# Kernel optimization log

Hardware: AMD Instinct MI355X
Metric: run time of the kernel (lower is better)

The kernel has to match this reference:

```python
import jax, jax.numpy as jnp
import numpy as np

EPS = 1e-5  # torch BatchNorm1d / LayerNorm default eps
B, S, CTX, C, H = 64, 31, 2048, 512, 8  # S must be num_particles+1 = 31
DH = C // H


def layernorm(x, g, b):
    mu = x.mean(-1, keepdims=True)
    var = x.var(-1, keepdims=True)
    return (x - mu) / jnp.sqrt(var + EPS) * g + b


def setup_inputs() -> dict:
    key = jax.random.key(0)
    ks = jax.random.split(key, 16)
    w = lambda k, shape: jax.random.normal(k, shape, jnp.float32) * 0.02
    return {
        "queries": jax.random.normal(ks[0], (B, S, C), jnp.float32),
        "contexts": jax.random.normal(ks[1], (B, CTX, C), jnp.float32),
        # SelfAttention params (BatchNorm1d(C) in training mode, q/k/v no bias, out with bias)
        "sa_bn_g": jnp.ones((C,), jnp.float32),
        "sa_bn_b": jnp.zeros((C,), jnp.float32),
        "sa_q_w": w(ks[2], (C, C)),
        "sa_k_w": w(ks[3], (C, C)),
        "sa_v_w": w(ks[4], (C, C)),
        "sa_out_w": w(ks[5], (C, C)),
        "sa_out_b": jnp.zeros((C,), jnp.float32),
        "sa_pre_g": jnp.ones((S * S,), jnp.float32),  # BatchNorm1d(961) on energy
        "sa_pre_b": jnp.zeros((S * S,), jnp.float32),
        # Cross Attention params (LayerNorm on queries, q/k/v no bias, out with bias)
        "ca_ln_g": jnp.ones((C,), jnp.float32),
        "ca_ln_b": jnp.zeros((C,), jnp.float32),
        "ca_q_w": w(ks[6], (C, C)),
        "ca_k_w": w(ks[7], (C, C)),
        "ca_v_w": w(ks[8], (C, C)),
        "ca_out_w": w(ks[9], (C, C)),
        "ca_out_b": jnp.zeros((C,), jnp.float32),
        # FFN: LN -> SiLU -> Linear(C,2C,no bias) -> LN -> SiLU -> Linear(2C,C,no bias)
        "ff_ln1_g": jnp.ones((C,), jnp.float32),
        "ff_ln1_b": jnp.zeros((C,), jnp.float32),
        "ff_w1": w(ks[10], (2 * C, C)),
        "ff_ln2_g": jnp.ones((2 * C,), jnp.float32),
        "ff_ln2_b": jnp.zeros((2 * C,), jnp.float32),
        "ff_w2": w(ks[11], (C, 2 * C)),
    }


def reference(queries, contexts, sa_bn_g, sa_bn_b, sa_q_w, sa_k_w, sa_v_w,
              sa_out_w, sa_out_b, sa_pre_g, sa_pre_b, ca_ln_g, ca_ln_b,
              ca_q_w, ca_k_w, ca_v_w, ca_out_w, ca_out_b, ff_ln1_g, ff_ln1_b,
              ff_w1, ff_ln2_g, ff_ln2_b, ff_w2):
    scale = jnp.sqrt(jnp.asarray(C, queries.dtype))

    # ---- SelfAttention (normalization='Batch', training-mode batch stats) ----
    mu = queries.mean(axis=(0, 1))            # per-channel over (B, S)
    var = queries.var(axis=(0, 1))
    xn = (queries - mu) / jnp.sqrt(var + EPS) * sa_bn_g + sa_bn_b
    q = jnp.einsum('bsc,oc->bso', xn, sa_q_w).reshape(B, S, H, DH)
    k = jnp.einsum('bsc,oc->bso', xn, sa_k_w).reshape(B, S, H, DH)
    v = jnp.einsum('bsc,oc->bso', xn, sa_v_w).reshape(B, S, H, DH)
    energy = jnp.einsum('nqhc,nkhc->nhqk', q, k)          # (B,H,S,S)
    # pre-softmax BatchNorm1d over channels = flattened (q,k) positions, batch dims = (B, H)
    e = energy.reshape(B, H, S * S)                        # (B,H,S*S)
    mu2 = e.mean(axis=(0, 1))
    var2 = e.var(axis=(0, 1))
    en = (e - mu2) / jnp.sqrt(var2 + EPS) * sa_pre_g + sa_pre_b
    energy_post = en.reshape(B, H, S, S)
    attn = jax.nn.softmax(energy_post / scale, axis=-1)
    o = jnp.einsum('nhql,nlhc->nqhc', attn, v).reshape(B, S, C)
    o = jnp.einsum('bsc,oc->bso', o, sa_out_w) + sa_out_b
    x_sa = o + queries                                     # residual

    # ---- Cross Attention (LayerNorm on queries pre-projection) ----
    qn = layernorm(x_sa, ca_ln_g, ca_ln_b)
    q2 = jnp.einsum('bsc,oc->bso', qn, ca_q_w).reshape(B, S, H, DH)
    k2 = jnp.einsum('btc,oc->bto', contexts, ca_k_w).reshape(B, CTX, H, DH)
    v2 = jnp.einsum('btc,oc->bto', contexts, ca_v_w).reshape(B, CTX, H, DH)
    energy2 = jnp.einsum('nqhc,nkhc->nhqk', q2, k2)        # (B,H,S,CTX)
    attn2 = jax.nn.softmax(energy2 / scale, axis=-1)
    o2 = jnp.einsum('nhql,nlhc->nqhc', attn2, v2).reshape(B, S, C)
    o2 = jnp.einsum('bsc,oc->bso', o2, ca_out_w) + ca_out_b
    x_ca = o2 + x_sa                                       # residual (queries_pre)

    # ---- FFN: LN -> SiLU -> Linear -> LN -> SiLU -> Linear, + residual ----
    h = jax.nn.silu(layernorm(x_ca, ff_ln1_g, ff_ln1_b))
    h = jnp.einsum('bsc,oc->bso', h, ff_w1)                # (B,S,2C)
    h = jax.nn.silu(layernorm(h, ff_ln2_g, ff_ln2_b))
    h = jnp.einsum('bsc,oc->bso', h, ff_w2)                # (B,S,C)
    out = x_ca + h                                         # dropout p=0.0 -> identity
    return out, energy2
```

## Files before the change

kernel.cpp:

```cpp
#include <hip/hip_runtime.h>
#include <hip/hip_bf16.h>
#include <cstdint>
#include <cstddef>

using u16 = unsigned short;
typedef short short8 __attribute__((ext_vector_type(8)));
typedef short short4v __attribute__((ext_vector_type(4)));
typedef float f32x4  __attribute__((ext_vector_type(4)));

#define DEV static __device__ __forceinline__

DEV float b2f(u16 u){ union{ unsigned i; float f; } v; v.i = ((unsigned)u)<<16; return v.f; }
DEV u16 f2b(float f){
  unsigned i = __builtin_bit_cast(unsigned, f);
  unsigned r = (i + 0x7FFFu + ((i>>16)&1u)) >> 16;
  return (u16)r;
}
DEV f32x4 mfma16(short8 a, short8 b, f32x4 c){
  return __builtin_amdgcn_mfma_f32_16x16x32_bf16(a, b, c, 0, 0, 0);
}

constexpr int Bn=64, Sn=31, Tn=2048, Cn=512, Hn=8;
constexpr int Rn=Bn*Sn;
constexpr int BHn=Bn*Hn;
constexpr int HRn=Hn*Sn;
constexpr float EPSf=1e-5f;
constexpr float INV_SCALE=0.04419417382415922f;

__global__ void k_badorder(float* out){
  if(threadIdx.x==0) out[0]=2000.f;
}

struct Src8 { const float* p[8]; };
__global__ __launch_bounds__(256) void k_cvtall(Src8 s, u16* __restrict__ dst){
  int i = blockIdx.x*256 + threadIdx.x;
  int seg, j=i;
  if(j>=196608){ if(j>=262144){seg=7;j-=262144;} else {seg=6;j-=196608;} }
  else { seg=j>>15; j&=32767; }
  const float* src=s.p[seg];
  f32x4 a=*(const f32x4*)&src[(size_t)j*8];
  f32x4 b=*(const f32x4*)&src[(size_t)j*8+4];
  short8 o;
  #pragma unroll
  for(int q=0;q<4;++q){ o[q]=(short)f2b(a[q]); o[4+q]=(short)f2b(b[q]); }
  *(short8*)&dst[(size_t)i*8]=o;
}

__global__ __launch_bounds__(256) void k_bn1_partial(const float* __restrict__ q,
    float* __restrict__ ps, float* __restrict__ psq){
  int c = blockIdx.x*256 + threadIdx.x;
  int r0 = blockIdx.y*124;
  float s=0.f, sq=0.f;
  for(int r=r0; r<r0+124; ++r){ float v=q[(size_t)r*Cn+c]; s+=v; sq+=v*v; }
  ps [blockIdx.y*Cn+c]=s;
  psq[blockIdx.y*Cn+c]=sq;
}
__global__ __launch_bounds__(512) void k_bn1_final(const float* __restrict__ ps,
    const float* __restrict__ psq, const float* __restrict__ g,
    const float* __restrict__ b, float* __restrict__ scale, float* __restrict__ shift){
  int c = threadIdx.x;
  float s=0.f, sq=0.f;
  for(int i=0;i<16;++i){ s+=ps[i*Cn+c]; sq+=psq[i*Cn+c]; }
  float m = s/(float)Rn;
  float v = sq/(float)Rn - m*m;
  float rs = rsqrtf(v+EPSf);
  float sc = rs*g[c];
  scale[c]=sc; shift[c]=b[c]-m*sc;
}

__global__ __launch_bounds__(256) void k_qkv(
    const float* __restrict__ q, const float* __restrict__ scale,
    const float* __restrict__ shift,
    const u16* __restrict__ W0, const u16* __restrict__ W1, const u16* __restrict__ W2,
    u16* __restrict__ o0, u16* __restrict__ o1v, u16* __restrict__ o2v)
{
  __shared__ u16 As[64][72];
  __shared__ u16 Ws[64][72];
  const int z=blockIdx.z;
  const u16* W = (z==0)?W0:((z==1)?W1:W2);
  u16* out     = (z==0)?o0:((z==1)?o1v:o2v);
  const int t=threadIdx.x, w=t>>6, l=t&63;
  const int m0=blockIdx.x*64, n0=blockIdx.y*64;
  const int lr=l&15, lk=(l>>4)*8;
  f32x4 zero={0.f,0.f,0.f,0.f};
  f32x4 acc[4];
  #pragma unroll
  for(int i=0;i<4;++i) acc[i]=zero;
  const int row0=t>>3, c8=(t&7)*8;
  for(int k0=0;k0<Cn;k0+=64){
    f32x4 sc0=*(const f32x4*)&scale[k0+c8], sc1=*(const f32x4*)&scale[k0+c8+4];
    f32x4 sh0=*(const f32x4*)&shift[k0+c8], sh1=*(const f32x4*)&shift[k0+c8+4];
    f32x4 x00=*(const f32x4*)&q[(size_t)(m0+row0   )*Cn+k0+c8];
    f32x4 x01=*(const f32x4*)&q[(size_t)(m0+row0   )*Cn+k0+c8+4];
    f32x4 x10=*(const f32x4*)&q[(size_t)(m0+32+row0)*Cn+k0+c8];
    f32x4 x11=*(const f32x4*)&q[(size_t)(m0+32+row0)*Cn+k0+c8+4];
    short8 a0,a1;
    #pragma unroll
    for(int j=0;j<4;++j){
      a0[j]  =(short)f2b(fmaf(x00[j],sc0[j],sh0[j]));
      a0[4+j]=(short)f2b(fmaf(x01[j],sc1[j],sh1[j]));
      a1[j]  =(short)f2b(fmaf(x10[j],sc0[j],sh0[j]));
      a1[4+j]=(short)f2b(fmaf(x11[j],sc1[j],sh1[j]));
    }
    short8 w0=*(const short8*)&W[(size_t)(n0+row0   )*Cn + k0 + c8];
    short8 w1=*(const short8*)&W[(size_t)(n0+32+row0)*Cn + k0 + c8];
    __syncthreads();
    *(short8*)&As[row0   ][c8]=a0;
    *(short8*)&As[32+row0][c8]=a1;
    *(short8*)&Ws[row0   ][c8]=w0;
    *(short8*)&Ws[32+row0][c8]=w1;
    __syncthreads();
    #pragma unroll
    for(int ks=0;ks<64;ks+=32){
      short8 af=*(const short8*)&As[w*16+lr][ks+lk];
      #pragma unroll
      for(int nf=0;nf<4;++nf){
        short8 bf=*(const short8*)&Ws[nf*16+lr][ks+lk];
        acc[nf]=mfma16(af,bf,acc[nf]);
      }
    }
  }
  const int r0=w*16+(l>>4)*4;
  #pragma unroll
  for(int nf=0;nf<4;++nf){
    const int n=n0+nf*16+lr;
    #pragma unroll
    for(int r=0;r<4;++r){
      const int m=m0+r0+r;
      out[(size_t)m*Cn+n]=f2b(acc[nf][r]);
    }
  }
}

template<bool F32OUT, bool RES32>
__global__ __launch_bounds__(256) void k_gemm64(
    const u16* __restrict__ A, const u16* __restrict__ W,
    const float* __restrict__ bias, const void* __restrict__ res,
    void* __restrict__ outv, int M, int N, int K)
{
  __shared__ u16 As[64][72];
  __shared__ u16 Ws[64][72];
  const int t=threadIdx.x, w=t>>6, l=t&63;
  const int m0=blockIdx.x*64, n0=blockIdx.y*64;
  const int lr=l&15, lk=(l>>4)*8;
  f32x4 zero={0.f,0.f,0.f,0.f};
  f32x4 acc[4];
  #pragma unroll
  for(int i=0;i<4;++i) acc[i]=zero;
  const int row0=t>>3, c8=(t&7)*8;
  for(int k0=0;k0<K;k0+=64){
    short8 a0=*(const short8*)&A[(size_t)(m0+row0   )*K + k0 + c8];
    short8 a1=*(const short8*)&A[(size_t)(m0+32+row0)*K + k0 + c8];
    short8 w0=*(const short8*)&W[(size_t)(n0+row0   )*K + k0 + c8];
    short8 w1=*(const short8*)&W[(size_t)(n0+32+row0)*K + k0 + c8];
    __syncthreads();
    *(short8*)&As[row0   ][c8]=a0;
    *(short8*)&As[32+row0][c8]=a1;
    *(short8*)&Ws[row0   ][c8]=w0;
    *(short8*)&Ws[32+row0][c8]=w1;
    __syncthreads();
    #pragma unroll
    for(int ks=0;ks<64;ks+=32){
      short8 af=*(const short8*)&As[w*16+lr][ks+lk];
      #pragma unroll
      for(int nf=0;nf<4;++nf){
        short8 bf=*(const short8*)&Ws[nf*16+lr][ks+lk];
        acc[nf]=mfma16(af,bf,acc[nf]);
      }
    }
  }
  const int r0=w*16+(l>>4)*4;
  #pragma unroll
  for(int nf=0;nf<4;++nf){
    const int n=n0+nf*16+lr;
    float bv = bias? bias[n] : 0.f;
    #pragma unroll
    for(int r=0;r<4;++r){
      const int m=m0+r0+r;
      float vv=acc[nf][r]+bv;
      if(res){
        if(RES32) vv += ((const float*)res)[(size_t)m*N+n];
        else      vv += b2f(((const u16*)res)[(size_t)m*N+n]);
      }
      if(F32OUT) ((float*)outv)[(size_t)m*N+n]=vv;
      else       ((u16*)outv)[(size_t)m*N+n]=f2b(vv);
    }
  }
}

__global__ __launch_bounds__(64) void k_energy1(const u16* __restrict__ q,
    const u16* __restrict__ k, float* __restrict__ e1){
  __shared__ u16 qs[32][72];
  __shared__ u16 ks_[32][72];
  const int bh=blockIdx.x, b=bh>>3, h=bh&7;
  const int t=threadIdx.x, l=t;
  #pragma unroll
  for(int i=0;i<4;++i){
    int flat=i*64+t; int row=flat>>3, c8=(flat&7)*8;
    short8 zq={0,0,0,0,0,0,0,0}, zk={0,0,0,0,0,0,0,0};
    if(row<31){
      zq=*(const short8*)&q[(size_t)(b*31+row)*Cn + h*64 + c8];
      zk=*(const short8*)&k[(size_t)(b*31+row)*Cn + h*64 + c8];
    }
    *(short8*)&qs [row][c8]=zq;
    *(short8*)&ks_[row][c8]=zk;
  }
  __syncthreads();
  const int lr=l&15, lk=(l>>4)*8;
  f32x4 zero={0.f,0.f,0.f,0.f};
  f32x4 acc[2][2];
  acc[0][0]=zero; acc[0][1]=zero; acc[1][0]=zero; acc[1][1]=zero;
  #pragma unroll
  for(int ks=0;ks<64;ks+=32){
    short8 a0=*(const short8*)&qs [lr   ][ks+lk];
    short8 a1=*(const short8*)&qs [16+lr][ks+lk];
    short8 b0=*(const short8*)&ks_[lr   ][ks+lk];
    short8 b1=*(const short8*)&ks_[16+lr][ks+lk];
    acc[0][0]=mfma16(a0,b0,acc[0][0]);
    acc[0][1]=mfma16(a0,b1,acc[0][1]);
    acc[1][0]=mfma16(a1,b0,acc[1][0]);
    acc[1][1]=mfma16(a1,b1,acc[1][1]);
  }
  const int r0=(l>>4)*4;
  #pragma unroll
  for(int i=0;i<2;++i)
    #pragma unroll
    for(int j=0;j<2;++j)
      #pragma unroll
      for(int r=0;r<4;++r){
        int qi=i*16+r0+r, ki=j*16+lr;
        if(qi<31 && ki<31) e1[(size_t)bh*961 + qi*31 + ki]=acc[i][j][r];
      }
}

__global__ __launch_bounds__(256) void k_bn2_partial(const float* __restrict__ e1,
    float* __restrict__ ps, float* __restrict__ psq){
  int p=blockIdx.x*256+threadIdx.x;
  if(p>=961) return;
  int r0=blockIdx.y*64;
  float s=0.f, sq=0.f;
  for(int r=r0;r<r0+64;++r){ float v=e1[(size_t)r*961+p]; s+=v; sq+=v*v; }
  ps [blockIdx.y*961+p]=s;
  psq[blockIdx.y*961+p]=sq;
}
__global__ __launch_bounds__(1024) void k_bn2_final(const float* __restrict__ ps,
    const float* __restrict__ psq, float* __restrict__ mu2, float* __restrict__ rstd2){
  int p=threadIdx.x; if(p>=961) return;
  float s=0.f, sq=0.f;
  for(int i=0;i<8;++i){ s+=ps[i*961+p]; sq+=psq[i*961+p]; }
  float m=s/512.f, v=sq/512.f-m*m;
  mu2[p]=m; rstd2[p]=rsqrtf(v+EPSf);
}

__global__ __launch_bounds__(256) void k_softmax_sa(const float* __restrict__ e1,
    const float* __restrict__ mu2, const float* __restrict__ rstd2,
    const float* __restrict__ g2, const float* __restrict__ bb2, u16* __restrict__ attn){
  int gidx=blockIdx.x*256+threadIdx.x;
  int bh=gidx/31, qi=gidx-bh*31;
  const float* er = e1 + (size_t)bh*961 + qi*31;
  float lg[31]; float mx=-1e30f;
  #pragma unroll
  for(int kk=0;kk<31;++kk){
    int p=qi*31+kk;
    float en=(er[kk]-mu2[p])*rstd2[p]*g2[p]+bb2[p];
    lg[kk]=en*INV_SCALE;
    mx=fmaxf(mx,lg[kk]);
  }
  float s=0.f;
  #pragma unroll
  for(int kk=0;kk<31;++kk){ lg[kk]=expf(lg[kk]-mx); s+=lg[kk]; }
  float inv=1.f/s;
  u16* ar = attn + (size_t)bh*1024 + qi*32;
  #pragma unroll
  for(int kk=0;kk<31;++kk) ar[kk]=f2b(lg[kk]*inv);
  ar[31]=0;
}

__global__ __launch_bounds__(64) void k_pv_sa(const u16* __restrict__ attn,
    const u16* __restrict__ v, u16* __restrict__ o1){
  __shared__ u16 vs[64][40];
  const int bh=blockIdx.x, b=bh>>3, h=bh&7;
  const int l=threadIdx.x;
  for(int kv=0;kv<31;++kv) vs[l][kv]=v[(size_t)(b*31+kv)*Cn + h*64 + l];
  vs[l][31]=0;
  __syncthreads();
  const int lr=l&15, lk=(l>>4)*8;
  f32x4 zero={0.f,0.f,0.f,0.f};
  f32x4 acc[2][4];
  #pragma unroll
  for(int i=0;i<2;++i)
    #pragma unroll
    for(int nf=0;nf<4;++nf) acc[i][nf]=zero;
  short8 a0=*(const short8*)&attn[(size_t)bh*1024 + lr*32 + lk];
  short8 a1=*(const short8*)&attn[(size_t)bh*1024 + (16+lr)*32 + lk];
  #pragma unroll
  for(int nf=0;nf<4;++nf){
    short8 bf=*(const short8*)&vs[nf*16+lr][lk];
    acc[0][nf]=mfma16(a0,bf,acc[0][nf]);
    acc[1][nf]=mfma16(a1,bf,acc[1][nf]);
  }
  const int r0=(l>>4)*4;
  #pragma unroll
  for(int i=0;i<2;++i)
    #pragma unroll
    for(int nf=0;nf<4;++nf)
      #pragma unroll
      for(int r=0;r<4;++r){
        int qi=i*16+r0+r;
        if(qi<31){
          int dh=nf*16+lr;
          o1[(size_t)(b*31+qi)*Cn + h*64 + dh]=f2b(acc[i][nf][r]);
        }
      }
}

template<int Wd, bool SILU>
__global__ __launch_bounds__(256) void k_ln(const u16* __restrict__ x,
    const float* __restrict__ g, const float* __restrict__ b, u16* __restrict__ out){
  const int w=threadIdx.x>>6, l=threadIdx.x&63;
  const int row=blockIdx.x*4+w;
  constexpr int NC=Wd/512;
  float v[NC*8];
  #pragma unroll
  for(int i=0;i<NC;++i){
    short8 s=*(const short8*)&x[(size_t)row*Wd + i*512 + l*8];
    #pragma unroll
    for(int j=0;j<8;++j) v[i*8+j]=b2f((u16)s[j]);
  }
  float s1=0.f, s2=0.f;
  #pragma unroll
  for(int e=0;e<NC*8;++e){ s1+=v[e]; s2+=v[e]*v[e]; }
  #pragma unroll
  for(int off=1;off<64;off<<=1){ s1+=__shfl_xor(s1,off,64); s2+=__shfl_xor(s2,off,64); }
  float m=s1/(float)Wd, var=s2/(float)Wd-m*m, rs=rsqrtf(var+EPSf);
  #pragma unroll
  for(int i=0;i<NC;++i){
    short8 o;
    #pragma unroll
    for(int j=0;j<8;++j){
      int c=i*512+l*8+j;
      float y=(v[i*8+j]-m)*rs*g[c]+b[c];
      if(SILU) y=y/(1.f+expf(-y));
      o[j]=(short)f2b(y);
    }
    *(short8*)&out[(size_t)row*Wd + i*512 + l*8]=o;
  }
}

__global__ __launch_bounds__(256) void k_qk(const u16* __restrict__ q2,
    const float* __restrict__ Wk, u16* __restrict__ qk){
  __shared__ u16 qs[32][72];
  __shared__ u16 bt[128][72];
  const int bh=blockIdx.x, b=bh>>3, h=bh&7;
  const int t=threadIdx.x, w=t>>6, l=t&63;
  {
    int row=t>>3, c8=(t&7)*8;
    short8 z={0,0,0,0,0,0,0,0};
    if(row<31) z=*(const short8*)&q2[(size_t)(b*31+row)*Cn + h*64 + c8];
    *(short8*)&qs[row][c8]=z;
  }
  const int lr=l&15, lk=(l>>4)*8;
  const int r0=(l>>4)*4;
  for(int nc=0;nc<512;nc+=128){
    __syncthreads();
    #pragma unroll
    for(int i=0;i<8;++i){
      int g=i*256+t;
      int d=g>>5, c4=(g&31)*4;
      f32x4 v=*(const f32x4*)&Wk[(size_t)(h*64+d)*Cn + nc + c4];
      #pragma unroll
      for(int jj=0;jj<4;++jj) bt[c4+jj][d]=f2b(v[jj]);
    }
    __syncthreads();
    f32x4 zero={0.f,0.f,0.f,0.f};
    f32x4 acc[2][2];
    acc[0][0]=zero; acc[0][1]=zero; acc[1][0]=zero; acc[1][1]=zero;
    #pragma unroll
    for(int ks=0;ks<64;ks+=32){
      short8 a0=*(const short8*)&qs[lr   ][ks+lk];
      short8 a1=*(const short8*)&qs[16+lr][ks+lk];
      #pragma unroll
      for(int nf=0;nf<2;++nf){
        short8 bf=*(const short8*)&bt[w*32+nf*16+lr][ks+lk];
        acc[0][nf]=mfma16(a0,bf,acc[0][nf]);
        acc[1][nf]=mfma16(a1,bf,acc[1][nf]);
      }
    }
    #pragma unroll
    for(int i=0;i<2;++i)
      #pragma unroll
      for(int nf=0;nf<2;++nf)
        #pragma unroll
        for(int r=0;r<4;++r){
          int qi=i*16+r0+r;
          if(qi<31)
            qk[((size_t)b*HRn + h*31 + qi)*Cn + nc + w*32 + nf*16 + lr]=f2b(acc[i][nf][r]);
        }
  }
}

__global__ __launch_bounds__(512) void k_e2big(const u16* __restrict__ qk,
    const float* __restrict__ ctx, float* __restrict__ e2, u16* __restrict__ ctxb){
  __shared__ u16 As[256][72];
  __shared__ u16 Bs[128][72];
  const int tb=blockIdx.x*128, b=blockIdx.y;
  const int t=threadIdx.x, w=t>>6, l=t&63;
  const int lr=l&15, lk=(l>>4)*8;
  const int wr=(w>>1)*64, wc=(w&1)*64;
  f32x4 zero={0.f,0.f,0.f,0.f};
  f32x4 acc[4][4];
  #pragma unroll
  for(int i=0;i<4;++i)
    #pragma unroll
    for(int j=0;j<4;++j) acc[i][j]=zero;
  for(int k0=0;k0<512;k0+=64){
    __syncthreads();
    #pragma unroll
    for(int i=0;i<4;++i){
      int g=i*512+t; int row=g>>3, c8=(g&7)*8;
      short8 z={0,0,0,0,0,0,0,0};
      if(row<HRn) z=*(const short8*)&qk[((size_t)b*HRn+row)*Cn + k0 + c8];
      *(short8*)&As[row][c8]=z;
    }
    #pragma unroll
    for(int i=0;i<4;++i){
      int g=i*512+t; int row=g>>4, c4=(g&15)*4;
      f32x4 v=*(const f32x4*)&ctx[((size_t)b*Tn + tb + row)*Cn + k0 + c4];
      short4v o;
      #pragma unroll
      for(int jj=0;jj<4;++jj) o[jj]=(short)f2b(v[jj]);
      *(short4v*)&Bs[row][c4]=o;
      *(short4v*)&ctxb[((size_t)b*Tn + tb + row)*Cn + k0 + c4]=o;
    }
    __syncthreads();
    #pragma unroll
    for(int ks=0;ks<64;ks+=32){
      short8 af[4], bf[4];
      #pragma unroll
      for(int i=0;i<4;++i){
        af[i]=*(const short8*)&As[wr+i*16+lr][ks+lk];
        bf[i]=*(const short8*)&Bs[wc+i*16+lr][ks+lk];
      }
      #pragma unroll
      for(int i=0;i<4;++i)
        #pragma unroll
        for(int j=0;j<4;++j)
          acc[i][j]=mfma16(af[i],bf[j],acc[i][j]);
    }
  }
  const int r0=(l>>4)*4;
  #pragma unroll
  for(int i=0;i<4;++i)
    #pragma unroll
    for(int j=0;j<4;++j)
      #pragma unroll
      for(int r=0;r<4;++r){
        int rm=wr+i*16+r0+r;
        if(rm<HRn)
          e2[((size_t)b*HRn+rm)*Tn + tb + wc + j*16 + lr]=acc[i][j][r];
      }
}

__global__ __launch_bounds__(256) void k_pstats(const float* __restrict__ e2,
    u16* __restrict__ pb, float* __restrict__ st){
  const int w=threadIdx.x>>6, l=threadIdx.x&63;
  const int gi=blockIdx.x*4+w;
  const int b=gi>>8, m=gi&255;
  u16* pr = pb + ((size_t)b*256+m)*2048;
  if(m>=HRn){
    short8 z={0,0,0,0,0,0,0,0};
    #pragma unroll
    for(int i=0;i<4;++i) *(short8*)&pr[i*512 + l*8]=z;
    return;
  }
  const float* er = e2 + ((size_t)b*HRn+m)*Tn;
  float v[32];
  #pragma unroll
  for(int i=0;i<4;++i){
    f32x4 a=*(const f32x4*)&er[i*512 + l*8];
    f32x4 c=*(const f32x4*)&er[i*512 + l*8 + 4];
    #pragma unroll
    for(int j=0;j<4;++j){ v[i*8+j]=a[j]*INV_SCALE; v[i*8+4+j]=c[j]*INV_SCALE; }
  }
  float mx=v[0];
  #pragma unroll
  for(int e=1;e<32;++e) mx=fmaxf(mx,v[e]);
  #pragma unroll
  for(int off=1;off<64;off<<=1) mx=fmaxf(mx,__shfl_xor(mx,off,64));
  float s=0.f;
  #pragma unroll
  for(int e=0;e<32;++e){ v[e]=expf(v[e]-mx); s+=v[e]; }
  #pragma unroll
  for(int off=1;off<64;off<<=1) s+=__shfl_xor(s,off,64);
  #pragma unroll
  for(int i=0;i<4;++i){
    short8 o;
    #pragma unroll
    for(int j=0;j<8;++j) o[j]=(short)f2b(v[i*8+j]);
    *(short8*)&pr[i*512 + l*8]=o;
  }
  if(l==0){ st[2*((size_t)b*HRn+m)]=mx; st[2*((size_t)b*HRn+m)+1]=s; }
}

__global__ __launch_bounds__(512) void k_pv2(const u16* __restrict__ pb,
    const u16* __restrict__ ctxb, const float* __restrict__ st,
    u16* __restrict__ o2t){
  __shared__ u16 As[128][72];
  __shared__ u16 Bs[128][76];
  const int n0=blockIdx.x*128, m0=blockIdx.y*128, b=blockIdx.z;
  const int t=threadIdx.x, w=t>>6, l=t&63;
  const int lr=l&15, lk=(l>>4)*8;
  const int wm=(w>>2)*64, wn=(w&3)*32;
  f32x4 zero={0.f,0.f,0.f,0.f};
  f32x4 acc[4][2];
  #pragma unroll
  for(int i=0;i<4;++i){ acc[i][0]=zero; acc[i][1]=zero; }
  const int arow=t>>3, ac8=(t&7)*8;
  const int bc=t&127, bq=(t>>7)*4;
  for(int kb=0;kb<Tn;kb+=64){
    __syncthreads();
    #pragma unroll
    for(int i=0;i<2;++i){
      int row=arow+i*64;
      *(short8*)&As[row][ac8] =
        *(const short8*)&pb[((size_t)b*256 + m0 + row)*Tn + kb + ac8];
    }
    #pragma unroll
    for(int i=0;i<4;++i){
      int kt0=(bq+i)*4;
      short4v o;
      #pragma unroll
      for(int jj=0;jj<4;++jj)
        o[jj]=(short)ctxb[((size_t)b*Tn + kb + kt0 + jj)*Cn + n0 + bc];
      *(short4v*)&Bs[bc][kt0]=o;
    }
    __syncthreads();
    #pragma unroll
    for(int ks=0;ks<64;ks+=32){
      short8 af[4], bf[2];
      #pragma unroll
      for(int i=0;i<4;++i)
        af[i]=*(const short8*)&As[wm+i*16+lr][ks+lk];
      #pragma unroll
      for(int j=0;j<2;++j){
        const u16* p=&Bs[wn+j*16+lr][ks+lk];
        short4v lo=*(const short4v*)p;
        short4v hi=*(const short4v*)(p+4);
        short8 bb;
        #pragma unroll
        for(int jj=0;jj<4;++jj){ bb[jj]=lo[jj]; bb[4+jj]=hi[jj]; }
        bf[j]=bb;
      }
      #pragma unroll
      for(int i=0;i<4;++i)
        #pragma unroll
        for(int j=0;j<2;++j)
          acc[i][j]=mfma16(af[i],bf[j],acc[i][j]);
    }
  }
  const int r0=(l>>4)*4;
  #pragma unroll
  for(int i=0;i<4;++i)
    #pragma unroll
    for(int j=0;j<2;++j)
      #pragma unroll
      for(int r=0;r<4;++r){
        int rm=m0+wm+i*16+r0+r;
        if(rm<HRn){
          float inv=1.f/st[2*((size_t)b*HRn+rm)+1];
          o2t[((size_t)b*HRn+rm)*Cn + n0+wn+j*16+lr]=f2b(acc[i][j][r]*inv);
        }
      }
}

__global__ __launch_bounds__(256) void k_o2proj(const u16* __restrict__ o2t,
    const float* __restrict__ Wv, u16* __restrict__ o2b){
  __shared__ u16 As[32][72];
  __shared__ u16 Ws[64][72];
  const int bh=blockIdx.x, b=bh>>3, h=bh&7;
  const int t=threadIdx.x, w=t>>6, l=t&63;
  const int lr=l&15, lk=(l>>4)*8;
  f32x4 zero={0.f,0.f,0.f,0.f};
  f32x4 acc[2]; acc[0]=zero; acc[1]=zero;
  for(int k0=0;k0<512;k0+=64){
    __syncthreads();
    {
      int row=t>>3, c8=(t&7)*8;
      short8 z={0,0,0,0,0,0,0,0};
      if(row<31) z=*(const short8*)&o2t[((size_t)b*HRn + h*31 + row)*Cn + k0 + c8];
      *(short8*)&As[row][c8]=z;
    }
    #pragma unroll
    for(int i=0;i<4;++i){
      int g=i*256+t; int row=g>>4, c4=(g&15)*4;
      f32x4 v=*(const f32x4*)&Wv[(size_t)(h*64+row)*Cn + k0 + c4];
      short4v o;
      #pragma unroll
      for(int jj=0;jj<4;++jj) o[jj]=(short)f2b(v[jj]);
      *(short4v*)&Ws[row][c4]=o;
    }
    __syncthreads();
    #pragma unroll
    for(int ks=0;ks<64;ks+=32){
      short8 a0=*(const short8*)&As[lr   ][ks+lk];
      short8 a1=*(const short8*)&As[16+lr][ks+lk];
      short8 bf=*(const short8*)&Ws[w*16+lr][ks+lk];
      acc[0]=mfma16(a0,bf,acc[0]);
      acc[1]=mfma16(a1,bf,acc[1]);
    }
  }
  const int r0=(l>>4)*4;
  #pragma unroll
  for(int i=0;i<2;++i)
    #pragma unroll
    for(int r=0;r<4;++r){
      int qi=i*16+r0+r;
      if(qi<31)
        o2b[((size_t)b*31+qi)*Cn + h*64 + w*16 + lr]=f2b(acc[i][r]);
    }
}

extern "C" void kernel_launch(void* const* d_in, const int* in_sizes, int n_in,
                              void* d_out, int out_size, void* d_ws, size_t ws_size,
                              hipStream_t stream){
  (void)out_size; (void)ws_size;
  float* outp=(float*)d_out;
  float* e2  =outp + (size_t)Rn*Cn;
  if(n_in<24 || in_sizes[0]!=Rn*Cn || in_sizes[1]!=Bn*Tn*Cn ||
     in_sizes[4]!=Cn*Cn || in_sizes[9]!=961 || in_sizes[20]!=2*Cn*Cn){
    k_badorder<<<1,64,0,stream>>>(outp);
    return;
  }
  const float* queries =(const float*)d_in[0];
  const float* contexts=(const float*)d_in[1];
  const float* sa_bn_g =(const float*)d_in[2];
  const float* sa_bn_b =(const float*)d_in[3];
  const float* sa_q_w  =(const float*)d_in[4];
  const float* sa_k_w  =(const float*)d_in[5];
  const float* sa_v_w  =(const float*)d_in[6];
  const float* sa_out_w=(const float*)d_in[7];
  const float* sa_out_b=(const float*)d_in[8];
  const float* sa_pre_g=(const float*)d_in[9];
  const float* sa_pre_b=(const float*)d_in[10];
  const float* ca_ln_g =(const float*)d_in[11];
  const float* ca_ln_b =(const float*)d_in[12];
  const float* ca_q_w  =(const float*)d_in[13];
  const float* ca_k_w  =(const float*)d_in[14];
  const float* ca_v_w  =(const float*)d_in[15];
  const float* ca_out_w=(const float*)d_in[16];
  const float* ca_out_b=(const float*)d_in[17];
  const float* ff_ln1_g=(const float*)d_in[18];
  const float* ff_ln1_b=(const float*)d_in[19];
  const float* ff_w1   =(const float*)d_in[20];
  const float* ff_ln2_g=(const float*)d_in[21];
  const float* ff_ln2_b=(const float*)d_in[22];
  const float* ff_w2   =(const float*)d_in[23];

  char* ws=(char*)d_ws;
  size_t off=0;
  auto alloc=[&](size_t bytes)->char*{
    char* p=ws+off; off=(off+bytes+255)&~(size_t)255; return p;
  };
  float* ps1  =(float*)alloc(16*Cn*4);
  float* psq1 =(float*)alloc(16*Cn*4);
  float* scale1=(float*)alloc(Cn*4);
  float* shift1=(float*)alloc(Cn*4);
  u16* w_sq=(u16*)alloc((size_t)Cn*Cn*2);
  u16* w_sk=(u16*)alloc((size_t)Cn*Cn*2);
  u16* w_sv=(u16*)alloc((size_t)Cn*Cn*2);
  u16* w_so=(u16*)alloc((size_t)Cn*Cn*2);
  u16* w_cq=(u16*)alloc((size_t)Cn*Cn*2);
  u16* w_co=(u16*)alloc((size_t)Cn*Cn*2);
  u16* w_f1=(u16*)alloc((size_t)2*Cn*Cn*2);
  u16* w_f2=(u16*)alloc((size_t)2*Cn*Cn*2);
  u16* qb  =(u16*)alloc((size_t)Rn*Cn*2);
  u16* kb  =(u16*)alloc((size_t)Rn*Cn*2);
  u16* vb  =(u16*)alloc((size_t)Rn*Cn*2);
  float* e1  =(float*)alloc((size_t)BHn*961*4);
  float* ps2 =(float*)alloc(8*961*4);
  float* psq2=(float*)alloc(8*961*4);
  float* mu2 =(float*)alloc(961*4);
  float* rstd2=(float*)alloc(961*4);
  u16* attn1=(u16*)alloc((size_t)BHn*1024*2);
  u16* o1  =(u16*)alloc((size_t)Rn*Cn*2);
  u16* xsa =(u16*)alloc((size_t)Rn*Cn*2);
  u16* qn  =(u16*)alloc((size_t)Rn*Cn*2);
  u16* q2b =(u16*)alloc((size_t)Rn*Cn*2);
  u16* qk  =(u16*)alloc((size_t)Bn*HRn*Cn*2);
  float* st=(float*)alloc((size_t)BHn*31*2*4);
  u16* o2b =(u16*)alloc((size_t)Rn*Cn*2);
  u16* xca =(u16*)alloc((size_t)Rn*Cn*2);
  u16* pb  =(u16*)alloc((size_t)Bn*256*Tn*2);
  u16* ctxb=(u16*)alloc((size_t)Bn*Tn*Cn*2);
  u16* o2t = qk;
  u16* f1  = o1;
  u16* t1  = qb;
  u16* f2  = vb;

  dim3 blk256(256), blk64(64), blk512(512);
  dim3 g64(Rn/64, Cn/64);

  Src8 s8; s8.p[0]=sa_q_w; s8.p[1]=sa_k_w; s8.p[2]=sa_v_w; s8.p[3]=sa_out_w;
  s8.p[4]=ca_q_w; s8.p[5]=ca_out_w; s8.p[6]=ff_w1; s8.p[7]=ff_w2;
  k_cvtall<<<1280,blk256,0,stream>>>(s8, w_sq);

  k_bn1_partial<<<dim3(2,16),blk256,0,stream>>>(queries, ps1, psq1);
  k_bn1_final<<<1,512,0,stream>>>(ps1,psq1,sa_bn_g,sa_bn_b,scale1,shift1);
  k_qkv<<<dim3(31,8,3),blk256,0,stream>>>(queries,scale1,shift1,w_sq,w_sk,w_sv,qb,kb,vb);
  k_energy1<<<BHn,blk64,0,stream>>>(qb,kb,e1);
  k_bn2_partial<<<dim3(4,8),blk256,0,stream>>>(e1,ps2,psq2);
  k_bn2_final<<<1,1024,0,stream>>>(ps2,psq2,mu2,rstd2);
  k_softmax_sa<<<62,blk256,0,stream>>>(e1,mu2,rstd2,sa_pre_g,sa_pre_b,attn1);
  k_pv_sa<<<BHn,blk64,0,stream>>>(attn1,vb,o1);
  k_gemm64<false,true><<<g64,blk256,0,stream>>>(o1,w_so,sa_out_b,queries,xsa,Rn,Cn,Cn);

  k_ln<512,false><<<Rn/4,blk256,0,stream>>>(xsa,ca_ln_g,ca_ln_b,qn);
  k_gemm64<false,false><<<g64,blk256,0,stream>>>(qn,w_cq,nullptr,nullptr,q2b,Rn,Cn,Cn);
  k_qk<<<BHn,blk256,0,stream>>>(q2b,ca_k_w,qk);
  k_e2big<<<dim3(Tn/128,Bn),blk512,0,stream>>>(qk,contexts,e2,ctxb);
  k_pstats<<<Bn*256/4,blk256,0,stream>>>(e2,pb,st);
  k_pv2<<<dim3(Cn/128,2,Bn),blk512,0,stream>>>(pb,ctxb,st,o2t);
  k_o2proj<<<BHn,blk256,0,stream>>>(o2t,ca_v_w,o2b);
  k_gemm64<false,false><<<g64,blk256,0,stream>>>(o2b,w_co,ca_out_b,xsa,xca,Rn,Cn,Cn);

  k_ln<512,true><<<Rn/4,blk256,0,stream>>>(xca,ff_ln1_g,ff_ln1_b,f1);
  k_gemm64<false,false><<<dim3(Rn/64,1024/64),blk256,0,stream>>>(f1,w_f1,nullptr,nullptr,t1,Rn,1024,Cn);
  k_ln<1024,true><<<Rn/4,blk256,0,stream>>>(t1,ff_ln2_g,ff_ln2_b,f2);
  k_gemm64<true,false><<<g64,blk256,0,stream>>>(f2,w_f2,nullptr,xca,outp,Rn,Cn,1024);
}
```

Measured before the change: 424.6 us.

## Fuse weight conversion with BN stats and softmax with PV, tune ctx loads

Merges the weight-to-bf16 conversion and BatchNorm partial statistics into one launch, and fuses the self-attention softmax into the PV kernel so attention probabilities stay in shared memory. Switches expf to __expf in the softmaxes and SiLU, makes the bf16 context copy a nontemporal store, and rewrites the transposed context load in the second PV kernel to use 32-bit reads of adjacent column pairs. These target launch overhead, an intermediate global buffer, and uncoalesced 16-bit loads. The fast exp slightly reduces accuracy, and the fused softmax runs on only 31 of 64 lanes.

```diff
diff --git a/kernel.cpp b/kernel.cpp
--- a/kernel.cpp
+++ b/kernel.cpp
@@ -32,29 +32,32 @@
 }
 
 struct Src8 { const float* p[8]; };
-__global__ __launch_bounds__(256) void k_cvtall(Src8 s, u16* __restrict__ dst){
-  int i = blockIdx.x*256 + threadIdx.x;
-  int seg, j=i;
-  if(j>=196608){ if(j>=262144){seg=7;j-=262144;} else {seg=6;j-=196608;} }
-  else { seg=j>>15; j&=32767; }
-  const float* src=s.p[seg];
-  f32x4 a=*(const f32x4*)&src[(size_t)j*8];
-  f32x4 b=*(const f32x4*)&src[(size_t)j*8+4];
-  short8 o;
-  #pragma unroll
-  for(int q=0;q<4;++q){ o[q]=(short)f2b(a[q]); o[4+q]=(short)f2b(b[q]); }
-  *(short8*)&dst[(size_t)i*8]=o;
-}
-
-__global__ __launch_bounds__(256) void k_bn1_partial(const float* __restrict__ q,
-    float* __restrict__ ps, float* __restrict__ psq){
-  int c = blockIdx.x*256 + threadIdx.x;
-  int r0 = blockIdx.y*124;
-  float s=0.f, sq=0.f;
-  for(int r=r0; r<r0+124; ++r){ float v=q[(size_t)r*Cn+c]; s+=v; sq+=v*v; }
-  ps [blockIdx.y*Cn+c]=s;
-  psq[blockIdx.y*Cn+c]=sq;
-}
+__global__ __launch_bounds__(256) void k_cvtbn(Src8 s, u16* __restrict__ dst,
+    const float* __restrict__ q, float* __restrict__ ps, float* __restrict__ psq){
+  int bid=blockIdx.x;
+  if(bid<1280){
+    int i = bid*256 + threadIdx.x;
+    int seg, j=i;
+    if(j>=196608){ if(j>=262144){seg=7;j-=262144;} else {seg=6;j-=196608;} }
+    else { seg=j>>15; j&=32767; }
+    const float* src=s.p[seg];
+    f32x4 a=*(const f32x4*)&src[(size_t)j*8];
+    f32x4 b=*(const f32x4*)&src[(size_t)j*8+4];
+    short8 o;
+    #pragma unroll
+    for(int qq=0;qq<4;++qq){ o[qq]=(short)f2b(a[qq]); o[4+qq]=(short)f2b(b[qq]); }
+    *(short8*)&dst[(size_t)i*8]=o;
+  } else {
+    int bb=bid-1280;
+    int c = (bb&1)*256 + threadIdx.x;
+    int r0 = (bb>>1)*124;
+    float sum=0.f, sq=0.f;
+    for(int r=r0;r<r0+124;++r){ float v=q[(size_t)r*Cn+c]; sum+=v; sq+=v*v; }
+    ps [(bb>>1)*Cn+c]=sum;
+    psq[(bb>>1)*Cn+c]=sq;
+  }
+}
+
 __global__ __launch_bounds__(512) void k_bn1_final(const float* __restrict__ ps,
     const float* __restrict__ psq, const float* __restrict__ g,
     const float* __restrict__ b, float* __restrict__ scale, float* __restrict__ shift){
@@ -252,37 +255,37 @@
   mu2[p]=m; rstd2[p]=rsqrtf(v+EPSf);
 }
 
-__global__ __launch_bounds__(256) void k_softmax_sa(const float* __restrict__ e1,
+__global__ __launch_bounds__(64) void k_smpv(const float* __restrict__ e1,
     const float* __restrict__ mu2, const float* __restrict__ rstd2,
-    const float* __restrict__ g2, const float* __restrict__ bb2, u16* __restrict__ attn){
-  int gidx=blockIdx.x*256+threadIdx.x;
-  int bh=gidx/31, qi=gidx-bh*31;
-  const float* er = e1 + (size_t)bh*961 + qi*31;
-  float lg[31]; float mx=-1e30f;
-  #pragma unroll
-  for(int kk=0;kk<31;++kk){
-    int p=qi*31+kk;
-    float en=(er[kk]-mu2[p])*rstd2[p]*g2[p]+bb2[p];
-    lg[kk]=en*INV_SCALE;
-    mx=fmaxf(mx,lg[kk]);
-  }
-  float s=0.f;
-  #pragma unroll
-  for(int kk=0;kk<31;++kk){ lg[kk]=expf(lg[kk]-mx); s+=lg[kk]; }
-  float inv=1.f/s;
-  u16* ar = attn + (size_t)bh*1024 + qi*32;
-  #pragma unroll
-  for(int kk=0;kk<31;++kk) ar[kk]=f2b(lg[kk]*inv);
-  ar[31]=0;
-}
-
-__global__ __launch_bounds__(64) void k_pv_sa(const u16* __restrict__ attn,
+    const float* __restrict__ g2, const float* __restrict__ bb2,
     const u16* __restrict__ v, u16* __restrict__ o1){
+  __shared__ u16 at[32][40];
   __shared__ u16 vs[64][40];
   const int bh=blockIdx.x, b=bh>>3, h=bh&7;
   const int l=threadIdx.x;
   for(int kv=0;kv<31;++kv) vs[l][kv]=v[(size_t)(b*31+kv)*Cn + h*64 + l];
   vs[l][31]=0;
+  if(l<31){
+    const float* er=e1+(size_t)bh*961 + l*31;
+    float lg[31]; float mx=-1e30f;
+    #pragma unroll
+    for(int kk=0;kk<31;++kk){
+      int p=l*31+kk;
+      float en=(er[kk]-mu2[p])*rstd2[p]*g2[p]+bb2[p];
+      lg[kk]=en*INV_SCALE;
+      mx=fmaxf(mx,lg[kk]);
+    }
+    float s=0.f;
+    #pragma unroll
+    for(int kk=0;kk<31;++kk){ lg[kk]=__expf(lg[kk]-mx); s+=lg[kk]; }
+    float inv=1.f/s;
+    #pragma unroll
+    for(int kk=0;kk<31;++kk) at[l][kk]=f2b(lg[kk]*inv);
+    at[l][31]=0;
+  } else if(l==31){
+    #pragma unroll
+    for(int kk=0;kk<32;++kk) at[31][kk]=0;
+  }
   __syncthreads();
   const int lr=l&15, lk=(l>>4)*8;
   f32x4 zero={0.f,0.f,0.f,0.f};
@@ -291,8 +294,8 @@
   for(int i=0;i<2;++i)
     #pragma unroll
     for(int nf=0;nf<4;++nf) acc[i][nf]=zero;
-  short8 a0=*(const short8*)&attn[(size_t)bh*1024 + lr*32 + lk];
-  short8 a1=*(const short8*)&attn[(size_t)bh*1024 + (16+lr)*32 + lk];
+  short8 a0=*(const short8*)&at[lr   ][lk];
+  short8 a1=*(const short8*)&at[16+lr][lk];
   #pragma unroll
   for(int nf=0;nf<4;++nf){
     short8 bf=*(const short8*)&vs[nf*16+lr][lk];
@@ -340,7 +343,7 @@
     for(int j=0;j<8;++j){
       int c=i*512+l*8+j;
       float y=(v[i*8+j]-m)*rs*g[c]+b[c];
-      if(SILU) y=y/(1.f+expf(-y));
+      if(SILU) y=y/(1.f+__expf(-y));
       o[j]=(short)f2b(y);
     }
     *(short8*)&out[(size_t)row*Wd + i*512 + l*8]=o;
@@ -430,7 +433,8 @@
       #pragma unroll
       for(int jj=0;jj<4;++jj) o[jj]=(short)f2b(v[jj]);
       *(short4v*)&Bs[row][c4]=o;
-      *(short4v*)&ctxb[((size_t)b*Tn + tb + row)*Cn + k0 + c4]=o;
+      __builtin_nontemporal_store(o,
+        (short4v*)&ctxb[((size_t)b*Tn + tb + row)*Cn + k0 + c4]);
     }
     __syncthreads();
     #pragma unroll
@@ -489,7 +493,7 @@
   for(int off=1;off<64;off<<=1) mx=fmaxf(mx,__shfl_xor(mx,off,64));
   float s=0.f;
   #pragma unroll
-  for(int e=0;e<32;++e){ v[e]=expf(v[e]-mx); s+=v[e]; }
+  for(int e=0;e<32;++e){ v[e]=__expf(v[e]-mx); s+=v[e]; }
   #pragma unroll
   for(int off=1;off<64;off<<=1) s+=__shfl_xor(s,off,64);
   #pragma unroll
@@ -516,7 +520,7 @@
   #pragma unroll
   for(int i=0;i<4;++i){ acc[i][0]=zero; acc[i][1]=zero; }
   const int arow=t>>3, ac8=(t&7)*8;
-  const int bc=t&127, bq=(t>>7)*4;
+  const int bc2=(t&63)*2, bg=t>>6;
   for(int kb=0;kb<Tn;kb+=64){
     __syncthreads();
     #pragma unroll
@@ -526,13 +530,17 @@
         *(const short8*)&pb[((size_t)b*256 + m0 + row)*Tn + kb + ac8];
     }
     #pragma unroll
-    for(int i=0;i<4;++i){
-      int kt0=(bq+i)*4;
-      short4v o;
-      #pragma unroll
-      for(int jj=0;jj<4;++jj)
-        o[jj]=(short)ctxb[((size_t)b*Tn + kb + kt0 + jj)*Cn + n0 + bc];
-      *(short4v*)&Bs[bc][kt0]=o;
+    for(int i=0;i<2;++i){
+      int r0 = bg*8 + i*4;
+      const u16* base=&ctxb[((size_t)b*Tn + kb + r0)*Cn + n0 + bc2];
+      unsigned v0=*(const unsigned*)(base);
+      unsigned v1=*(const unsigned*)(base + Cn);
+      unsigned v2=*(const unsigned*)(base + 2*Cn);
+      unsigned v3=*(const unsigned*)(base + 3*Cn);
+      short4v lo={(short)(v0&0xffffu),(short)(v1&0xffffu),(short)(v2&0xffffu),(short)(v3&0xffffu)};
+      short4v hi={(short)(v0>>16),(short)(v1>>16),(short)(v2>>16),(short)(v3>>16)};
+      *(short4v*)&Bs[bc2  ][r0]=lo;
+      *(short4v*)&Bs[bc2+1][r0]=hi;
     }
     __syncthreads();
     #pragma unroll
@@ -681,7 +689,6 @@
   float* psq2=(float*)alloc(8*961*4);
   float* mu2 =(float*)alloc(961*4);
   float* rstd2=(float*)alloc(961*4);
-  u16* attn1=(u16*)alloc((size_t)BHn*1024*2);
   u16* o1  =(u16*)alloc((size_t)Rn*Cn*2);
   u16* xsa =(u16*)alloc((size_t)Rn*Cn*2);
   u16* qn  =(u16*)alloc((size_t)Rn*Cn*2);
@@ -702,16 +709,14 @@
 
   Src8 s8; s8.p[0]=sa_q_w; s8.p[1]=sa_k_w; s8.p[2]=sa_v_w; s8.p[3]=sa_out_w;
   s8.p[4]=ca_q_w; s8.p[5]=ca_out_w; s8.p[6]=ff_w1; s8.p[7]=ff_w2;
-  k_cvtall<<<1280,blk256,0,stream>>>(s8, w_sq);
-
-  k_bn1_partial<<<dim3(2,16),blk256,0,stream>>>(queries, ps1, psq1);
+  k_cvtbn<<<1312,blk256,0,stream>>>(s8, w_sq, queries, ps1, psq1);
+
   k_bn1_final<<<1,512,0,stream>>>(ps1,psq1,sa_bn_g,sa_bn_b,scale1,shift1);
   k_qkv<<<dim3(31,8,3),blk256,0,stream>>>(queries,scale1,shift1,w_sq,w_sk,w_sv,qb,kb,vb);
   k_energy1<<<BHn,blk64,0,stream>>>(qb,kb,e1);
   k_bn2_partial<<<dim3(4,8),blk256,0,stream>>>(e1,ps2,psq2);
   k_bn2_final<<<1,1024,0,stream>>>(ps2,psq2,mu2,rstd2);
-  k_softmax_sa<<<62,blk256,0,stream>>>(e1,mu2,rstd2,sa_pre_g,sa_pre_b,attn1);
-  k_pv_sa<<<BHn,blk64,0,stream>>>(attn1,vb,o1);
+  k_smpv<<<BHn,blk64,0,stream>>>(e1,mu2,rstd2,sa_pre_g,sa_pre_b,vb,o1);
   k_gemm64<false,true><<<g64,blk256,0,stream>>>(o1,w_so,sa_out_b,queries,xsa,Rn,Cn,Cn);
 
   k_ln<512,false><<<Rn/4,blk256,0,stream>>>(xsa,ca_ln_g,ca_ln_b,qn);
```

New measurement: 440.2 us. 1.04x slower.
